# Kernel tuning notes

Hardware: AMD Instinct MI355X
Metric: run time of the kernel (lower is better)

Reference implementation:

```python
import jax, jax.numpy as jnp
import numpy as np

N_NODES = 50000
N_EDGES = 400000
NUM_FEATURES = 32
NUM_GRAPHS = 64
NUM_CLASSES = 2


def setup_inputs() -> dict:
    key = jax.random.key(0)
    ks = jax.random.split(key, 24)
    inp = {
        "x": jax.random.normal(ks[0], (N_NODES, NUM_FEATURES), dtype=jnp.float32),
        "edge_index": jax.random.randint(ks[1], (2, N_EDGES), 0, N_NODES),
        "edge_attr": jax.random.uniform(ks[2], (N_EDGES, 1), dtype=jnp.float32),
        "batch": jnp.sort(jax.random.randint(ks[3], (N_NODES,), 0, NUM_GRAPHS)),
        # nn1: Linear(1,10) -> ReLU -> Linear(10, 32*16)
        "nn1_w1": jax.random.normal(ks[4], (1, 10), dtype=jnp.float32) * 0.3,
        "nn1_b1": jnp.zeros((10,), jnp.float32),
        "nn1_w2": jax.random.normal(ks[5], (10, NUM_FEATURES * 16), dtype=jnp.float32) * 0.1,
        "nn1_b2": jnp.zeros((NUM_FEATURES * 16,), jnp.float32),
        "conv1_root": jax.random.normal(ks[6], (NUM_FEATURES, 16), dtype=jnp.float32) * 0.1,
        "conv1_bias": jnp.zeros((16,), jnp.float32),
        # nn2: Linear(1,10) -> ReLU -> Linear(10, 16*32)
        "nn2_w1": jax.random.normal(ks[7], (1, 10), dtype=jnp.float32) * 0.3,
        "nn2_b1": jnp.zeros((10,), jnp.float32),
        "nn2_w2": jax.random.normal(ks[8], (10, 16 * 32), dtype=jnp.float32) * 0.1,
        "nn2_b2": jnp.zeros((16 * 32,), jnp.float32),
        "conv2_root": jax.random.normal(ks[9], (16, 32), dtype=jnp.float32) * 0.15,
        "conv2_bias": jnp.zeros((32,), jnp.float32),
        "fc1_w": jax.random.normal(ks[10], (32, 64), dtype=jnp.float32) * 0.15,
        "fc1_b": jnp.zeros((64,), jnp.float32),
        "fc2_w": jax.random.normal(ks[11], (64, NUM_CLASSES), dtype=jnp.float32) * 0.1,
        "fc2_b": jnp.zeros((NUM_CLASSES,), jnp.float32),
    }
    return inp


def _nnconv(x, edge_src, edge_dst, edge_attr, w1, b1, w2, b2, root, bias, in_ch, out_ch):
    # Per-edge weight matrix from edge MLP: [E, in_ch, out_ch]
    h = jax.nn.relu(edge_attr @ w1 + b1) @ w2 + b2
    W = h.reshape(-1, in_ch, out_ch)
    msg = jnp.einsum('ei,eio->eo', x[edge_src], W)  # [E, out_ch]
    agg = jax.ops.segment_sum(msg, edge_dst, num_segments=N_NODES)
    cnt = jax.ops.segment_sum(jnp.ones((msg.shape[0],), x.dtype), edge_dst, num_segments=N_NODES)
    mean = agg / jnp.maximum(cnt, 1.0)[:, None]
    return mean + x @ root + bias


def reference(x, edge_index, edge_attr, batch,
              nn1_w1, nn1_b1, nn1_w2, nn1_b2, conv1_root, conv1_bias,
              nn2_w1, nn2_b1, nn2_w2, nn2_b2, conv2_root, conv2_bias,
              fc1_w, fc1_b, fc2_w, fc2_b):
    src, dst = edge_index[0], edge_index[1]
    h = jax.nn.elu(_nnconv(x, src, dst, edge_attr, nn1_w1, nn1_b1, nn1_w2, nn1_b2,
                           conv1_root, conv1_bias, NUM_FEATURES, 16))
    h = jax.nn.elu(_nnconv(h, src, dst, edge_attr, nn2_w1, nn2_b1, nn2_w2, nn2_b2,
                           conv2_root, conv2_bias, 16, 32))
    # global mean pool over graphs
    gsum = jax.ops.segment_sum(h, batch, num_segments=NUM_GRAPHS)
    gcnt = jax.ops.segment_sum(jnp.ones((h.shape[0],), h.dtype), batch, num_segments=NUM_GRAPHS)
    g = gsum / jnp.maximum(gcnt, 1.0)[:, None]
    g = jax.nn.elu(g @ fc1_w + fc1_b)
    return jax.nn.log_softmax(g @ fc2_w + fc2_b, axis=1)
```

## Files before the change

kernel.cpp:

```cpp
#include <hip/hip_runtime.h>
#include <math.h>

#define N_NODES 50000
#define N_EDGES 400000
#define F_IN 32
#define NUM_GRAPHS 64


__global__ __launch_bounds__(256) void k1_p1(const float* __restrict__ x,
        const float* __restrict__ w2, const float* __restrict__ b2,
        const float* __restrict__ root, float* __restrict__ P) {
    __shared__ float Wl[32][192];
    __shared__ float xl[16][32];
    int t = threadIdx.x;
    for (int idx = t; idx < 32 * 192; idx += 256) {
        int i = idx / 192, c = idx % 192;
        float w;
        if (c < 160)      { int j = c >> 4;  int o = c & 15;  w = w2[j * 512 + i * 16 + o]; }
        else if (c < 176) { int o = c - 160; w = b2[i * 16 + o]; }
        else              { int o = c - 176; w = root[i * 16 + o]; }
        Wl[i][c] = w;
    }
    int n0 = blockIdx.x * 16;
    for (int idx = t; idx < 16 * 32; idx += 256) {
        int nl = idx >> 5, i = idx & 31;
        int n = n0 + nl;
        xl[nl][i] = (n < N_NODES) ? x[n * 32 + i] : 0.f;
    }
    __syncthreads();
    int nl = t >> 4, cs = t & 15;
    int n = n0 + nl;
    if (n >= N_NODES) return;
    float acc[12];
#pragma unroll
    for (int k = 0; k < 12; k++) acc[k] = 0.f;
#pragma unroll
    for (int i = 0; i < 32; i++) {
        float xv = xl[nl][i];
#pragma unroll
        for (int k = 0; k < 12; k++) acc[k] += xv * Wl[i][cs + 16 * k];
    }
#pragma unroll
    for (int k = 0; k < 12; k++) P[(size_t)n * 192 + cs + 16 * k] = acc[k];
}

__global__ __launch_bounds__(256) void k4_p2(const float* __restrict__ h1,
        const float* __restrict__ w2, const float* __restrict__ b2,
        const float* __restrict__ root, float* __restrict__ P) {
    __shared__ float Wl[16][384];
    __shared__ float hl[16][16];
    int t = threadIdx.x;
    for (int idx = t; idx < 16 * 384; idx += 256) {
        int i = idx / 384, c = idx % 384;
        float w;
        if (c < 320)      { int j = c >> 5;  int o = c & 31;  w = w2[j * 512 + i * 32 + o]; }
        else if (c < 352) { int o = c - 320; w = b2[i * 32 + o]; }
        else              { int o = c - 352; w = root[i * 32 + o]; }
        Wl[i][c] = w;
    }
    int n0 = blockIdx.x * 16;
    for (int idx = t; idx < 16 * 16; idx += 256) {
        int nl = idx >> 4, i = idx & 15;
        int n = n0 + nl;
        hl[nl][i] = (n < N_NODES) ? h1[n * 16 + i] : 0.f;
    }
    __syncthreads();
    int nl = t >> 4, cs = t & 15;
    int n = n0 + nl;
    if (n >= N_NODES) return;
    float acc[24];
#pragma unroll
    for (int k = 0; k < 24; k++) acc[k] = 0.f;
#pragma unroll
    for (int i = 0; i < 16; i++) {
        float hv = hl[nl][i];
#pragma unroll
        for (int k = 0; k < 24; k++) acc[k] += hv * Wl[i][cs + 16 * k];
    }
#pragma unroll
    for (int k = 0; k < 24; k++) P[(size_t)n * 384 + cs + 16 * k] = acc[k];
}

__global__ __launch_bounds__(256) void k2_edge1(const float* __restrict__ P,
        const int* __restrict__ src, const int* __restrict__ dst,
        const float* __restrict__ ea, const float* __restrict__ w1,
        const float* __restrict__ b1, float* __restrict__ agg,
        float* __restrict__ cnt) {
    int t = threadIdx.x;
    int e = blockIdx.x * 16 + (t >> 4);
    int o = t & 15;
    if (e >= N_EDGES) return;
    float a = ea[e];
    int s = src[e], d = dst[e];
    const float* Pr = P + (size_t)s * 192;
    float m = Pr[160 + o];
#pragma unroll
    for (int j = 0; j < 10; j++) {
        float r = fmaxf(a * w1[j] + b1[j], 0.f);
        m += r * Pr[j * 16 + o];
    }
    atomicAdd(agg + d * 16 + o, m);
    if (o == 0) atomicAdd(cnt + d, 1.0f);
}

__global__ __launch_bounds__(256) void k5_edge2(const float* __restrict__ P,
        const int* __restrict__ src, const int* __restrict__ dst,
        const float* __restrict__ ea, const float* __restrict__ w1,
        const float* __restrict__ b1, float* __restrict__ agg) {
    int t = threadIdx.x;
    int e = blockIdx.x * 8 + (t >> 5);
    int o = t & 31;
    if (e >= N_EDGES) return;
    float a = ea[e];
    int s = src[e], d = dst[e];
    const float* Pr = P + (size_t)s * 384;
    float m = Pr[320 + o];
#pragma unroll
    for (int j = 0; j < 10; j++) {
        float r = fmaxf(a * w1[j] + b1[j], 0.f);
        m += r * Pr[j * 32 + o];
    }
    atomicAdd(agg + d * 32 + o, m);
}

__global__ void k3_node1(const float* __restrict__ agg, const float* __restrict__ cnt,
        const float* __restrict__ P, const float* __restrict__ bias,
        float* __restrict__ h1) {
    int gid = blockIdx.x * 256 + threadIdx.x;
    if (gid >= N_NODES * 16) return;
    int n = gid >> 4, o = gid & 15;
    float c = fmaxf(cnt[n], 1.0f);
    float v = agg[gid] / c + P[(size_t)n * 192 + 176 + o] + bias[o];
    h1[gid] = v > 0.f ? v : expm1f(v);
}

__global__ void k6_node2(const float* __restrict__ agg, const float* __restrict__ cnt,
        const float* __restrict__ P, const float* __restrict__ bias,
        float* __restrict__ h2) {
    int gid = blockIdx.x * 256 + threadIdx.x;
    if (gid >= N_NODES * 32) return;
    int n = gid >> 5, o = gid & 31;
    float c = fmaxf(cnt[n], 1.0f);
    float v = agg[gid] / c + P[(size_t)n * 384 + 352 + o] + bias[o];
    h2[gid] = v > 0.f ? v : expm1f(v);
}

__global__ __launch_bounds__(256) void k7_pool(const float* __restrict__ h2,
        const int* __restrict__ batch, float* __restrict__ gp) {
    int g = blockIdx.x;
    int t = threadIdx.x;
    int lo = 0, hi = N_NODES;
    while (lo < hi) { int mid = (lo + hi) >> 1; if (batch[mid] < g) lo = mid + 1; else hi = mid; }
    int start = lo;
    hi = N_NODES;
    while (lo < hi) { int mid = (lo + hi) >> 1; if (batch[mid] < g + 1) lo = mid + 1; else hi = mid; }
    int end = lo;
    int o = t & 31, ch = t >> 5;
    float s = 0.f;
    for (int n = start + ch; n < end; n += 8) s += h2[(size_t)n * 32 + o];
    __shared__ float red[8][32];
    red[ch][o] = s;
    __syncthreads();
    if (t < 32) {
        float tot = 0.f;
#pragma unroll
        for (int c = 0; c < 8; c++) tot += red[c][t];
        gp[g * 32 + t] = tot / fmaxf((float)(end - start), 1.0f);
    }
}

__global__ __launch_bounds__(256) void k8_head(const float* __restrict__ gp,
        const float* __restrict__ fc1w, const float* __restrict__ fc1b,
        const float* __restrict__ fc2w, const float* __restrict__ fc2b,
        float* __restrict__ out) {
    __shared__ float gl[64][32];
    __shared__ float w1l[32][64];
    __shared__ float hl[64][64];
    __shared__ float zl[64][2];
    int t = threadIdx.x;
    for (int idx = t; idx < 64 * 32; idx += 256) gl[idx >> 5][idx & 31] = gp[idx];
    for (int idx = t; idx < 32 * 64; idx += 256) w1l[idx >> 6][idx & 63] = fc1w[idx];
    __syncthreads();
    for (int idx = t; idx < 64 * 64; idx += 256) {
        int gg = idx >> 6, c = idx & 63;
        float acc = fc1b[c];
#pragma unroll
        for (int i = 0; i < 32; i++) acc += gl[gg][i] * w1l[i][c];
        hl[gg][c] = acc > 0.f ? acc : expm1f(acc);
    }
    __syncthreads();
    if (t < 128) {
        int gg = t >> 1, k = t & 1;
        float acc = fc2b[k];
#pragma unroll
        for (int c = 0; c < 64; c++) acc += hl[gg][c] * fc2w[c * 2 + k];
        zl[gg][k] = acc;
    }
    __syncthreads();
    if (t < 128) {
        int gg = t >> 1, k = t & 1;
        float z0 = zl[gg][0], z1 = zl[gg][1];
        float m = fmaxf(z0, z1);
        float lse = m + logf(expf(z0 - m) + expf(z1 - m));
        out[t] = zl[gg][k] - lse;
    }
}

extern "C" void kernel_launch(void* const* d_in, const int* in_sizes, int n_in,
                              void* d_out, int out_size, void* d_ws, size_t ws_size,
                              hipStream_t stream) {
    const float* x       = (const float*)d_in[0];
    const int*   ei      = (const int*)d_in[1];
    const float* ea      = (const float*)d_in[2];
    const int*   batch   = (const int*)d_in[3];
    const float* nn1_w1  = (const float*)d_in[4];
    const float* nn1_b1  = (const float*)d_in[5];
    const float* nn1_w2  = (const float*)d_in[6];
    const float* nn1_b2  = (const float*)d_in[7];
    const float* c1_root = (const float*)d_in[8];
    const float* c1_bias = (const float*)d_in[9];
    const float* nn2_w1  = (const float*)d_in[10];
    const float* nn2_b1  = (const float*)d_in[11];
    const float* nn2_w2  = (const float*)d_in[12];
    const float* nn2_b2  = (const float*)d_in[13];
    const float* c2_root = (const float*)d_in[14];
    const float* c2_bias = (const float*)d_in[15];
    const float* fc1w    = (const float*)d_in[16];
    const float* fc1b    = (const float*)d_in[17];
    const float* fc2w    = (const float*)d_in[18];
    const float* fc2b    = (const float*)d_in[19];
    const int* src = ei;
    const int* dst = ei + N_EDGES;

    float* ws = (float*)d_ws;
    size_t off = 0;
    float* P    = ws + off; off += (size_t)N_NODES * 384;
    float* cnt  = ws + off; off += N_NODES;
    float* agg1 = ws + off; off += (size_t)N_NODES * 16;
    float* agg2 = ws + off; off += (size_t)N_NODES * 32;
    float* h1   = ws + off; off += (size_t)N_NODES * 16;
    float* h2   = ws + off; off += (size_t)N_NODES * 32;
    float* gp   = ws + off; off += NUM_GRAPHS * 32;

    hipMemsetAsync(cnt, 0, (size_t)(N_NODES + N_NODES * 16) * sizeof(float), stream);
    hipMemsetAsync(agg2, 0, (size_t)N_NODES * 32 * sizeof(float), stream);

    k1_p1<<<(N_NODES + 15) / 16, 256, 0, stream>>>(x, nn1_w2, nn1_b2, c1_root, P);
    k2_edge1<<<(N_EDGES + 15) / 16, 256, 0, stream>>>(P, src, dst, ea, nn1_w1, nn1_b1, agg1, cnt);
    k3_node1<<<(N_NODES * 16 + 255) / 256, 256, 0, stream>>>(agg1, cnt, P, c1_bias, h1);
    k4_p2<<<(N_NODES + 15) / 16, 256, 0, stream>>>(h1, nn2_w2, nn2_b2, c2_root, P);
    k5_edge2<<<(N_EDGES + 7) / 8, 256, 0, stream>>>(P, src, dst, ea, nn2_w1, nn2_b1, agg2);
    k6_node2<<<(N_NODES * 32 + 255) / 256, 256, 0, stream>>>(agg2, cnt, P, c2_bias, h2);
    k7_pool<<<NUM_GRAPHS, 256, 0, stream>>>(h2, batch, gp);
    k8_head<<<1, 256, 0, stream>>>(gp, fc1w, fc1b, fc2w, fc2b, (float*)d_out);
}
```

Baseline: 333.5 us.

## Store per-node projections in fp16 and fuse node epilogues into consumers

Measured after the change: 353.0 us. 1.06x slower.

```diff
diff --git a/kernel.cpp b/kernel.cpp
--- a/kernel.cpp
+++ b/kernel.cpp
@@ -1,15 +1,15 @@
 #include <hip/hip_runtime.h>
+#include <hip/hip_fp16.h>
 #include <math.h>
 
 #define N_NODES 50000
 #define N_EDGES 400000
-#define F_IN 32
 #define NUM_GRAPHS 64
 
 
 __global__ __launch_bounds__(256) void k1_p1(const float* __restrict__ x,
         const float* __restrict__ w2, const float* __restrict__ b2,
-        const float* __restrict__ root, float* __restrict__ P) {
+        const float* __restrict__ root, __half* __restrict__ P) {
     __shared__ float Wl[32][192];
     __shared__ float xl[16][32];
     int t = threadIdx.x;
@@ -17,8 +17,8 @@
         int i = idx / 192, c = idx % 192;
         float w;
         if (c < 160)      { int j = c >> 4;  int o = c & 15;  w = w2[j * 512 + i * 16 + o]; }
-        else if (c < 176) { int o = c - 160; w = b2[i * 16 + o]; }
-        else              { int o = c - 176; w = root[i * 16 + o]; }
+        else if (c < 176) { w = b2[i * 16 + (c - 160)]; }
+        else              { w = root[i * 16 + (c - 176)]; }
         Wl[i][c] = w;
     }
     int n0 = blockIdx.x * 16;
@@ -28,25 +28,31 @@
         xl[nl][i] = (n < N_NODES) ? x[n * 32 + i] : 0.f;
     }
     __syncthreads();
-    int nl = t >> 4, cs = t & 15;
+    int nl = t >> 4, l = t & 15;
     int n = n0 + nl;
     if (n >= N_NODES) return;
-    float acc[12];
-#pragma unroll
-    for (int k = 0; k < 12; k++) acc[k] = 0.f;
+    float a0[6], a1[6];
+#pragma unroll
+    for (int k = 0; k < 6; k++) { a0[k] = 0.f; a1[k] = 0.f; }
 #pragma unroll
     for (int i = 0; i < 32; i++) {
         float xv = xl[nl][i];
 #pragma unroll
-        for (int k = 0; k < 12; k++) acc[k] += xv * Wl[i][cs + 16 * k];
-    }
-#pragma unroll
-    for (int k = 0; k < 12; k++) P[(size_t)n * 192 + cs + 16 * k] = acc[k];
-}
-
-__global__ __launch_bounds__(256) void k4_p2(const float* __restrict__ h1,
+        for (int k = 0; k < 6; k++) {
+            a0[k] += xv * Wl[i][2 * l + 32 * k];
+            a1[k] += xv * Wl[i][2 * l + 1 + 32 * k];
+        }
+    }
+    __half2* Po = (__half2*)(P + (size_t)n * 192);
+#pragma unroll
+    for (int k = 0; k < 6; k++) Po[l + 16 * k] = __floats2half2_rn(a0[k], a1[k]);
+}
+
+__global__ __launch_bounds__(256) void k4_p2(const float* __restrict__ agg1,
+        const float* __restrict__ cnt, const __half* __restrict__ P1,
+        const float* __restrict__ bias1,
         const float* __restrict__ w2, const float* __restrict__ b2,
-        const float* __restrict__ root, float* __restrict__ P) {
+        const float* __restrict__ root, __half* __restrict__ P2) {
     __shared__ float Wl[16][384];
     __shared__ float hl[16][16];
     int t = threadIdx.x;
@@ -54,99 +60,101 @@
         int i = idx / 384, c = idx % 384;
         float w;
         if (c < 320)      { int j = c >> 5;  int o = c & 31;  w = w2[j * 512 + i * 32 + o]; }
-        else if (c < 352) { int o = c - 320; w = b2[i * 32 + o]; }
-        else              { int o = c - 352; w = root[i * 32 + o]; }
+        else if (c < 352) { w = b2[i * 32 + (c - 320)]; }
+        else              { w = root[i * 32 + (c - 352)]; }
         Wl[i][c] = w;
     }
     int n0 = blockIdx.x * 16;
-    for (int idx = t; idx < 16 * 16; idx += 256) {
-        int nl = idx >> 4, i = idx & 15;
+    {
+        int nl = t >> 4, i = t & 15;
         int n = n0 + nl;
-        hl[nl][i] = (n < N_NODES) ? h1[n * 16 + i] : 0.f;
-    }
-    __syncthreads();
-    int nl = t >> 4, cs = t & 15;
+        float v = 0.f;
+        if (n < N_NODES) {
+            float c = fmaxf(cnt[n], 1.0f);
+            v = agg1[n * 16 + i] / c + __half2float(P1[(size_t)n * 192 + 176 + i]) + bias1[i];
+            v = v > 0.f ? v : expm1f(v);
+        }
+        hl[nl][i] = v;
+    }
+    __syncthreads();
+    int nl = t >> 4, l = t & 15;
     int n = n0 + nl;
     if (n >= N_NODES) return;
-    float acc[24];
-#pragma unroll
-    for (int k = 0; k < 24; k++) acc[k] = 0.f;
+    float a0[12], a1[12];
+#pragma unroll
+    for (int k = 0; k < 12; k++) { a0[k] = 0.f; a1[k] = 0.f; }
 #pragma unroll
     for (int i = 0; i < 16; i++) {
         float hv = hl[nl][i];
 #pragma unroll
-        for (int k = 0; k < 24; k++) acc[k] += hv * Wl[i][cs + 16 * k];
-    }
-#pragma unroll
-    for (int k = 0; k < 24; k++) P[(size_t)n * 384 + cs + 16 * k] = acc[k];
-}
-
-__global__ __launch_bounds__(256) void k2_edge1(const float* __restrict__ P,
+        for (int k = 0; k < 12; k++) {
+            a0[k] += hv * Wl[i][2 * l + 32 * k];
+            a1[k] += hv * Wl[i][2 * l + 1 + 32 * k];
+        }
+    }
+    __half2* Po = (__half2*)(P2 + (size_t)n * 384);
+#pragma unroll
+    for (int k = 0; k < 12; k++) Po[l + 16 * k] = __floats2half2_rn(a0[k], a1[k]);
+}
+
+__global__ __launch_bounds__(256) void k2_edge1(const __half* __restrict__ P,
         const int* __restrict__ src, const int* __restrict__ dst,
         const float* __restrict__ ea, const float* __restrict__ w1,
         const float* __restrict__ b1, float* __restrict__ agg,
         float* __restrict__ cnt) {
     int t = threadIdx.x;
-    int e = blockIdx.x * 16 + (t >> 4);
-    int o = t & 15;
+    int e = blockIdx.x * 32 + (t >> 3);
+    int l = t & 7;
     if (e >= N_EDGES) return;
     float a = ea[e];
     int s = src[e], d = dst[e];
-    const float* Pr = P + (size_t)s * 192;
-    float m = Pr[160 + o];
+    const __half2* Pr = (const __half2*)(P + (size_t)s * 192);
+    float r[10];
+#pragma unroll
+    for (int j = 0; j < 10; j++) r[j] = fmaxf(a * w1[j] + b1[j], 0.f);
+    float2 q = __half22float2(Pr[80 + l]);
+    float m0 = q.x, m1 = q.y;
 #pragma unroll
     for (int j = 0; j < 10; j++) {
-        float r = fmaxf(a * w1[j] + b1[j], 0.f);
-        m += r * Pr[j * 16 + o];
-    }
-    atomicAdd(agg + d * 16 + o, m);
-    if (o == 0) atomicAdd(cnt + d, 1.0f);
-}
-
-__global__ __launch_bounds__(256) void k5_edge2(const float* __restrict__ P,
+        float2 p = __half22float2(Pr[j * 8 + l]);
+        m0 += r[j] * p.x;
+        m1 += r[j] * p.y;
+    }
+    atomicAdd(agg + d * 16 + 2 * l, m0);
+    atomicAdd(agg + d * 16 + 2 * l + 1, m1);
+    if (l == 0) atomicAdd(cnt + d, 1.0f);
+}
+
+__global__ __launch_bounds__(256) void k5_edge2(const __half* __restrict__ P,
         const int* __restrict__ src, const int* __restrict__ dst,
         const float* __restrict__ ea, const float* __restrict__ w1,
         const float* __restrict__ b1, float* __restrict__ agg) {
     int t = threadIdx.x;
-    int e = blockIdx.x * 8 + (t >> 5);
-    int o = t & 31;
+    int e = blockIdx.x * 16 + (t >> 4);
+    int l = t & 15;
     if (e >= N_EDGES) return;
     float a = ea[e];
     int s = src[e], d = dst[e];
-    const float* Pr = P + (size_t)s * 384;
-    float m = Pr[320 + o];
+    const __half2* Pr = (const __half2*)(P + (size_t)s * 384);
+    float r[10];
+#pragma unroll
+    for (int j = 0; j < 10; j++) r[j] = fmaxf(a * w1[j] + b1[j], 0.f);
+    float2 q = __half22float2(Pr[160 + l]);
+    float m0 = q.x, m1 = q.y;
 #pragma unroll
     for (int j = 0; j < 10; j++) {
-        float r = fmaxf(a * w1[j] + b1[j], 0.f);
-        m += r * Pr[j * 32 + o];
-    }
-    atomicAdd(agg + d * 32 + o, m);
-}
-
-__global__ void k3_node1(const float* __restrict__ agg, const float* __restrict__ cnt,
-        const float* __restrict__ P, const float* __restrict__ bias,
-        float* __restrict__ h1) {
-    int gid = blockIdx.x * 256 + threadIdx.x;
-    if (gid >= N_NODES * 16) return;
-    int n = gid >> 4, o = gid & 15;
-    float c = fmaxf(cnt[n], 1.0f);
-    float v = agg[gid] / c + P[(size_t)n * 192 + 176 + o] + bias[o];
-    h1[gid] = v > 0.f ? v : expm1f(v);
-}
-
-__global__ void k6_node2(const float* __restrict__ agg, const float* __restrict__ cnt,
-        const float* __restrict__ P, const float* __restrict__ bias,
-        float* __restrict__ h2) {
-    int gid = blockIdx.x * 256 + threadIdx.x;
-    if (gid >= N_NODES * 32) return;
-    int n = gid >> 5, o = gid & 31;
-    float c = fmaxf(cnt[n], 1.0f);
-    float v = agg[gid] / c + P[(size_t)n * 384 + 352 + o] + bias[o];
-    h2[gid] = v > 0.f ? v : expm1f(v);
-}
-
-__global__ __launch_bounds__(256) void k7_pool(const float* __restrict__ h2,
-        const int* __restrict__ batch, float* __restrict__ gp) {
+        float2 p = __half22float2(Pr[j * 16 + l]);
+        m0 += r[j] * p.x;
+        m1 += r[j] * p.y;
+    }
+    atomicAdd(agg + d * 32 + 2 * l, m0);
+    atomicAdd(agg + d * 32 + 2 * l + 1, m1);
+}
+
+__global__ __launch_bounds__(256) void k7_pool(const float* __restrict__ agg2,
+        const float* __restrict__ cnt, const __half* __restrict__ P2,
+        const float* __restrict__ bias2, const int* __restrict__ batch,
+        float* __restrict__ gp) {
     int g = blockIdx.x;
     int t = threadIdx.x;
     int lo = 0, hi = N_NODES;
@@ -157,7 +165,12 @@
     int end = lo;
     int o = t & 31, ch = t >> 5;
     float s = 0.f;
-    for (int n = start + ch; n < end; n += 8) s += h2[(size_t)n * 32 + o];
+    for (int n = start + ch; n < end; n += 8) {
+        float c = fmaxf(cnt[n], 1.0f);
+        float v = agg2[(size_t)n * 32 + o] / c
+                + __half2float(P2[(size_t)n * 384 + 352 + o]) + bias2[o];
+        s += v > 0.f ? v : expm1f(v);
+    }
     __shared__ float red[8][32];
     red[ch][o] = s;
     __syncthreads();
@@ -232,25 +245,21 @@
     const int* src = ei;
     const int* dst = ei + N_EDGES;
 
-    float* ws = (float*)d_ws;
-    size_t off = 0;
-    float* P    = ws + off; off += (size_t)N_NODES * 384;
-    float* cnt  = ws + off; off += N_NODES;
-    float* agg1 = ws + off; off += (size_t)N_NODES * 16;
-    float* agg2 = ws + off; off += (size_t)N_NODES * 32;
-    float* h1   = ws + off; off += (size_t)N_NODES * 16;
-    float* h2   = ws + off; off += (size_t)N_NODES * 32;
-    float* gp   = ws + off; off += NUM_GRAPHS * 32;
-
-    hipMemsetAsync(cnt, 0, (size_t)(N_NODES + N_NODES * 16) * sizeof(float), stream);
-    hipMemsetAsync(agg2, 0, (size_t)N_NODES * 32 * sizeof(float), stream);
-
-    k1_p1<<<(N_NODES + 15) / 16, 256, 0, stream>>>(x, nn1_w2, nn1_b2, c1_root, P);
-    k2_edge1<<<(N_EDGES + 15) / 16, 256, 0, stream>>>(P, src, dst, ea, nn1_w1, nn1_b1, agg1, cnt);
-    k3_node1<<<(N_NODES * 16 + 255) / 256, 256, 0, stream>>>(agg1, cnt, P, c1_bias, h1);
-    k4_p2<<<(N_NODES + 15) / 16, 256, 0, stream>>>(h1, nn2_w2, nn2_b2, c2_root, P);
-    k5_edge2<<<(N_EDGES + 7) / 8, 256, 0, stream>>>(P, src, dst, ea, nn2_w1, nn2_b1, agg2);
-    k6_node2<<<(N_NODES * 32 + 255) / 256, 256, 0, stream>>>(agg2, cnt, P, c2_bias, h2);
-    k7_pool<<<NUM_GRAPHS, 256, 0, stream>>>(h2, batch, gp);
+    char* ws = (char*)d_ws;
+    __half* P1 = (__half*)ws;
+    __half* P2 = (__half*)(ws + (size_t)N_NODES * 192 * 2);
+    float* fbase = (float*)(ws + (size_t)N_NODES * 192 * 2 + (size_t)N_NODES * 384 * 2);
+    float* cnt  = fbase;
+    float* agg1 = cnt + N_NODES;
+    float* agg2 = agg1 + (size_t)N_NODES * 16;
+    float* gp   = agg2 + (size_t)N_NODES * 32;
+
+    hipMemsetAsync(cnt, 0, (size_t)(N_NODES + N_NODES * 16 + N_NODES * 32) * sizeof(float), stream);
+
+    k1_p1<<<(N_NODES + 15) / 16, 256, 0, stream>>>(x, nn1_w2, nn1_b2, c1_root, P1);
+    k2_edge1<<<(N_EDGES + 31) / 32, 256, 0, stream>>>(P1, src, dst, ea, nn1_w1, nn1_b1, agg1, cnt);
+    k4_p2<<<(N_NODES + 15) / 16, 256, 0, stream>>>(agg1, cnt, P1, c1_bias, nn2_w2, nn2_b2, c2_root, P2);
+    k5_edge2<<<(N_EDGES + 15) / 16, 256, 0, stream>>>(P2, src, dst, ea, nn2_w1, nn2_b1, agg2);
+    k7_pool<<<NUM_GRAPHS, 256, 0, stream>>>(agg2, cnt, P2, c2_bias, batch, gp);
     k8_head<<<1, 256, 0, stream>>>(gp, fc1w, fc1b, fc2w, fc2b, (float*)d_out);
 }
```
